# Kernel optimization log

Measured on AMD Instinct MI355X. Metric: run time of the kernel, lower is better.

The kernel has to match this reference:

```python
import jax, jax.numpy as jnp
import numpy as np

D_MODEL = 512
WINDOW = 128
N_HEADS = 8


def setup_inputs() -> dict:
    key = jax.random.key(0)
    k1, k2, k3, k4, k5 = jax.random.split(key, 5)
    B, S, D = 8, 4096, D_MODEL
    scale = 1.0 / np.sqrt(D)
    return {
        "x": jax.random.normal(k1, (B, S, D), dtype=jnp.float32),
        "in_proj_w": jax.random.normal(k2, (3 * D, D), dtype=jnp.float32) * scale,
        "in_proj_b": jax.random.normal(k3, (3 * D,), dtype=jnp.float32) * 0.02,
        "out_proj_w": jax.random.normal(k4, (D, D), dtype=jnp.float32) * scale,
        "out_proj_b": jax.random.normal(k5, (D,), dtype=jnp.float32) * 0.02,
    }


def reference(x, in_proj_w, in_proj_b, out_proj_w, out_proj_b):
    # Non-overlapping sliding-window MHA with shared weights per window.
    B, S, D = x.shape
    W = WINDOW
    H = N_HEADS
    hd = D // H
    nw = S // W  # S chosen divisible by window size

    xw = x.reshape(B, nw, W, D)
    # Fused QKV projection (torch in_proj_weight layout: [3D, D], y = x @ W^T + b)
    qkv = jnp.einsum("bnwd,ed->bnwe", xw, in_proj_w) + in_proj_b  # [B,nw,W,3D]
    q, k, v = jnp.split(qkv, 3, axis=-1)

    def to_heads(t):
        return t.reshape(B, nw, W, H, hd)

    q = to_heads(q) * (1.0 / np.sqrt(hd))
    k = to_heads(k)
    v = to_heads(v)

    # Block-diagonal attention: scores only within each window [B,nw,H,W,W]
    scores = jnp.einsum("bnqhd,bnkhd->bnhqk", q, k)
    attn = jax.nn.softmax(scores, axis=-1)
    ctx = jnp.einsum("bnhqk,bnkhd->bnqhd", attn, v)  # [B,nw,W,H,hd]
    ctx = ctx.reshape(B, S, D)

    out = jnp.einsum("bsd,ed->bse", ctx, out_proj_w) + out_proj_b
    return out
```

## Files before the change

### kernel.cpp

```cpp
#include <hip/hip_runtime.h>


typedef __bf16 bf16x8 __attribute__((ext_vector_type(8)));
typedef __bf16 bf16x4 __attribute__((ext_vector_type(4)));
typedef float  f32x4  __attribute__((ext_vector_type(4)));

#define MFMA16(a, b, c) __builtin_amdgcn_mfma_f32_16x16x32_bf16((a), (b), (c), 0, 0, 0)
#define VMCNT_(n) asm volatile("s_waitcnt vmcnt(" #n ")" ::: "memory")
#define VMCNT(n) VMCNT_(n)
#define LGKM0() asm volatile("s_waitcnt lgkmcnt(0)" ::: "memory")

__device__ __forceinline__ void gload_lds16(const __bf16* g, void* l) {
    __builtin_amdgcn_global_load_lds(
        (const __attribute__((address_space(1))) unsigned int*)g,
        (__attribute__((address_space(3))) unsigned int*)l, 16, 0, 0);
}

__device__ __forceinline__ void cvt8(const float* __restrict__ s,
                                     __bf16* __restrict__ d, long i) {
    const float4* s4 = reinterpret_cast<const float4*>(s);
    float4 a = s4[2 * i], b = s4[2 * i + 1];
    bf16x8 v;
    v[0] = (__bf16)a.x; v[1] = (__bf16)a.y; v[2] = (__bf16)a.z; v[3] = (__bf16)a.w;
    v[4] = (__bf16)b.x; v[5] = (__bf16)b.y; v[6] = (__bf16)b.z; v[7] = (__bf16)b.w;
    *reinterpret_cast<bf16x8*>(d + 8 * i) = v;
}

__global__ void convert_k(const float* __restrict__ x,
                          const float* __restrict__ w_in,
                          const float* __restrict__ w_out,
                          __bf16* __restrict__ x_bf,
                          __bf16* __restrict__ w_in_bf,
                          __bf16* __restrict__ w_out_bf)
{
    long i0 = (long)blockIdx.x * blockDim.x + threadIdx.x;
    long stride = (long)gridDim.x * blockDim.x;
    for (long i = i0; i < 16777216 / 8; i += stride) cvt8(x, x_bf, i);
    for (long i = i0; i < 786432 / 8;   i += stride) cvt8(w_in, w_in_bf, i);
    for (long i = i0; i < 262144 / 8;   i += stride) cvt8(w_out, w_out_bf, i);
}

template<int EPI, int NN>
__global__ __launch_bounds__(512, 2)
void gemm256(const __bf16* __restrict__ A,
             const __bf16* __restrict__ Bw,
             const float* __restrict__ bias,
             void* __restrict__ Cq,
             __bf16* __restrict__ vT)
{
    __shared__ __align__(16) char smem[65536];

    const int nwg = gridDim.x;
    const int chunk = nwg >> 3;
    const int bid = blockIdx.x;
    const int wg = (bid & 7) * chunk + (bid >> 3);
    const int nidx = wg % NN;
    const int midx = wg / NN;
    const long mbase = (long)midx * 256;
    const int colbase = nidx * 256;

    const int tid = threadIdx.x;
    const int w = tid >> 6, lane = tid & 63;
    const int lrow = lane & 15, hi = lane >> 4;
    const int wm = w >> 2, wn = w & 3;

    const int srow = tid >> 2;
    const int kchunk = (tid & 3) ^ ((srow >> 1) & 3);
    const __bf16* PA = A  + (mbase + srow) * 512 + kchunk * 8;
    const __bf16* PB = Bw + ((long)colbase + srow) * 512 + kchunk * 8;
    const int rd16 = (hi ^ ((lrow >> 1) & 3)) << 4;

    auto stage = [&](int t) {
        char* Ab = smem + (t & 1) * 16384;
        char* Bb = smem + 32768 + (t & 1) * 16384;
        const int ko = t * 32;
        gload_lds16(PA + ko,             Ab + w * 1024);
        gload_lds16(PA + 128 * 512 + ko, Ab + 8192 + w * 1024);
        gload_lds16(PB + ko,             Bb + w * 1024);
        gload_lds16(PB + 128 * 512 + ko, Bb + 8192 + w * 1024);
    };

    f32x4 acc[8][4];
    #pragma unroll
    for (int rt = 0; rt < 8; ++rt)
        #pragma unroll
        for (int ct = 0; ct < 4; ++ct) acc[rt][ct] = (f32x4){0.f, 0.f, 0.f, 0.f};

    stage(0);

    #pragma unroll 1
    for (int t = 0; t < 16; ++t) {
        VMCNT(0);
        LGKM0();
        __builtin_amdgcn_s_barrier();
        if (t < 15) stage(t + 1);
        const char* Ab = smem + (t & 1) * 16384;
        const char* Bb = smem + 32768 + (t & 1) * 16384;
        bf16x8 af[4], bfr[4];
        #pragma unroll
        for (int ct = 0; ct < 4; ++ct)
            bfr[ct] = *reinterpret_cast<const bf16x8*>(
                Bb + (64 * wn + 16 * ct + lrow) * 64 + rd16);
        #pragma unroll
        for (int i = 0; i < 4; ++i)
            af[i] = *reinterpret_cast<const bf16x8*>(
                Ab + (128 * wm + 16 * i + lrow) * 64 + rd16);
        __builtin_amdgcn_s_setprio(1);
        #pragma unroll
        for (int i = 0; i < 4; ++i)
            #pragma unroll
            for (int ct = 0; ct < 4; ++ct)
                acc[i][ct] = MFMA16(af[i], bfr[ct], acc[i][ct]);
        __builtin_amdgcn_s_setprio(0);
        #pragma unroll
        for (int i = 0; i < 4; ++i)
            af[i] = *reinterpret_cast<const bf16x8*>(
                Ab + (128 * wm + 64 + 16 * i + lrow) * 64 + rd16);
        __builtin_amdgcn_s_setprio(1);
        #pragma unroll
        for (int i = 0; i < 4; ++i)
            #pragma unroll
            for (int ct = 0; ct < 4; ++ct)
                acc[4 + i][ct] = MFMA16(af[i], bfr[ct], acc[4 + i][ct]);
        __builtin_amdgcn_s_setprio(0);
    }

    if (EPI == 0) {
        if (colbase < 1024) {
            const float scale = (colbase < 512) ? 0.125f : 1.0f;
            __bf16* qk = (__bf16*)Cq;
            #pragma unroll
            for (int ct = 0; ct < 4; ++ct) {
                int colg = colbase + 64 * wn + 16 * ct + lrow;
                float b = bias[colg];
                #pragma unroll
                for (int rt = 0; rt < 8; ++rt) {
                    long row = mbase + 128 * wm + 16 * rt + 4 * hi;
                    #pragma unroll
                    for (int r = 0; r < 4; ++r)
                        qk[(row + r) * 1024 + colg] = (__bf16)((acc[rt][ct][r] + b) * scale);
                }
            }
        } else {
            #pragma unroll
            for (int ct = 0; ct < 4; ++ct) {
                int colg = colbase + 64 * wn + 16 * ct + lrow;
                float b = bias[colg];
                int e2 = colg - 1024;
                int h = e2 >> 6, d = e2 & 63;
                #pragma unroll
                for (int rt = 0; rt < 8; ++rt) {
                    long row = mbase + 128 * wm + 16 * rt + 4 * hi;
                    int win = (int)(row >> 7), tok0 = (int)(row & 127);
                    bf16x4 pk;
                    pk[0] = (__bf16)(acc[rt][ct][0] + b);
                    pk[1] = (__bf16)(acc[rt][ct][1] + b);
                    pk[2] = (__bf16)(acc[rt][ct][2] + b);
                    pk[3] = (__bf16)(acc[rt][ct][3] + b);
                    *reinterpret_cast<bf16x4*>(
                        vT + (((long)win * 8 + h) * 64 + d) * 128 + tok0) = pk;
                }
            }
        }
    } else {
        float* outp = (float*)Cq;
        #pragma unroll
        for (int ct = 0; ct < 4; ++ct) {
            int colg = colbase + 64 * wn + 16 * ct + lrow;
            float b = bias[colg];
            #pragma unroll
            for (int rt = 0; rt < 8; ++rt) {
                long row = mbase + 128 * wm + 16 * rt + 4 * hi;
                #pragma unroll
                for (int r = 0; r < 4; ++r)
                    outp[(row + r) * 512 + colg] = acc[rt][ct][r] + b;
            }
        }
    }
}

__global__ __launch_bounds__(256)
void swa_attn(const __bf16* __restrict__ qk,
              const __bf16* __restrict__ vT,
              __bf16* __restrict__ ctx)
{
    __shared__ __bf16 p_lds[4][32][136];

    const int bid = blockIdx.x;
    const int win = bid >> 3, h = bid & 7;
    const int tid = threadIdx.x;
    const int w = tid >> 6, lane = tid & 63;
    const int lrow = lane & 15, hi = lane >> 4;
    const long tokb = (long)win * 128;

    bf16x8 qa[2][2];
    #pragma unroll
    for (int rt = 0; rt < 2; ++rt)
        #pragma unroll
        for (int ks = 0; ks < 2; ++ks)
            qa[rt][ks] = *reinterpret_cast<const bf16x8*>(
                qk + (tokb + 32 * w + 16 * rt + lrow) * 1024 + h * 64 + ks * 32 + hi * 8);

    f32x4 s[2][8];
    #pragma unroll
    for (int rt = 0; rt < 2; ++rt)
        #pragma unroll
        for (int ct = 0; ct < 8; ++ct) s[rt][ct] = (f32x4){0.f, 0.f, 0.f, 0.f};
    #pragma unroll
    for (int ks = 0; ks < 2; ++ks) {
        #pragma unroll
        for (int ct = 0; ct < 8; ++ct) {
            bf16x8 kb = *reinterpret_cast<const bf16x8*>(
                qk + (tokb + 16 * ct + lrow) * 1024 + 512 + h * 64 + ks * 32 + hi * 8);
            s[0][ct] = MFMA16(qa[0][ks], kb, s[0][ct]);
            s[1][ct] = MFMA16(qa[1][ks], kb, s[1][ct]);
        }
    }

    float inv[2][4];
    #pragma unroll
    for (int rt = 0; rt < 2; ++rt) {
        #pragma unroll
        for (int r = 0; r < 4; ++r) {
            float m = s[rt][0][r];
            #pragma unroll
            for (int ct = 1; ct < 8; ++ct) m = fmaxf(m, s[rt][ct][r]);
            m = fmaxf(m, __shfl_xor(m, 1));
            m = fmaxf(m, __shfl_xor(m, 2));
            m = fmaxf(m, __shfl_xor(m, 4));
            m = fmaxf(m, __shfl_xor(m, 8));
            float sum = 0.f;
            #pragma unroll
            for (int ct = 0; ct < 8; ++ct) {
                float e = __expf(s[rt][ct][r] - m);
                sum += e;
                p_lds[w][16 * rt + 4 * hi + r][16 * ct + lrow] = (__bf16)e;
            }
            sum += __shfl_xor(sum, 1);
            sum += __shfl_xor(sum, 2);
            sum += __shfl_xor(sum, 4);
            sum += __shfl_xor(sum, 8);
            inv[rt][r] = 1.f / sum;
        }
    }

    f32x4 o[2][4];
    #pragma unroll
    for (int rt = 0; rt < 2; ++rt)
        #pragma unroll
        for (int ct = 0; ct < 4; ++ct) o[rt][ct] = (f32x4){0.f, 0.f, 0.f, 0.f};
    const __bf16* vb = vT + ((long)win * 8 + h) * 64 * 128;
    #pragma unroll
    for (int kt = 0; kt < 4; ++kt) {
        bf16x8 pa0 = *reinterpret_cast<const bf16x8*>(&p_lds[w][lrow][32 * kt + 8 * hi]);
        bf16x8 pa1 = *reinterpret_cast<const bf16x8*>(&p_lds[w][16 + lrow][32 * kt + 8 * hi]);
        #pragma unroll
        for (int ct = 0; ct < 4; ++ct) {
            bf16x8 vf = *reinterpret_cast<const bf16x8*>(
                vb + (16 * ct + lrow) * 128 + 32 * kt + 8 * hi);
            o[0][ct] = MFMA16(pa0, vf, o[0][ct]);
            o[1][ct] = MFMA16(pa1, vf, o[1][ct]);
        }
    }

    #pragma unroll
    for (int rt = 0; rt < 2; ++rt)
        #pragma unroll
        for (int ct = 0; ct < 4; ++ct)
            #pragma unroll
            for (int r = 0; r < 4; ++r) {
                long tok = tokb + 32 * w + 16 * rt + 4 * hi + r;
                ctx[tok * 512 + h * 64 + 16 * ct + lrow] =
                    (__bf16)(o[rt][ct][r] * inv[rt][r]);
            }
}

extern "C" void kernel_launch(void* const* d_in, const int* in_sizes, int n_in,
                              void* d_out, int out_size, void* d_ws, size_t ws_size,
                              hipStream_t stream)
{
    const float* x     = (const float*)d_in[0];
    const float* w_in  = (const float*)d_in[1];
    const float* b_in  = (const float*)d_in[2];
    const float* w_out = (const float*)d_in[3];
    const float* b_out = (const float*)d_in[4];

    char* ws = (char*)d_ws;
    __bf16* x_bf     = (__bf16*)(ws);
    __bf16* ctx      = (__bf16*)(ws);
    __bf16* vT       = (__bf16*)(ws + 33554432);
    __bf16* w_in_bf  = (__bf16*)(ws + 67108864);
    __bf16* w_out_bf = (__bf16*)(ws + 68681728);
    __bf16* qk       = (__bf16*)d_out;

    convert_k<<<2048, 256, 0, stream>>>(x, w_in, w_out, x_bf, w_in_bf, w_out_bf);
    gemm256<0, 6><<<768, 512, 0, stream>>>(x_bf, w_in_bf, b_in, (void*)qk, vT);
    swa_attn<<<2048, 256, 0, stream>>>(qk, vT, ctx);
    gemm256<1, 2><<<256, 512, 0, stream>>>(ctx, w_out_bf, b_out, d_out, nullptr);
}
```

Before: 165.9 us.

## Use 256x128 GEMM tiles with triple-buffered LDS and staged coalesced epilogue

Shrinks the GEMM workgroup to 256 threads with a 256x128 output tile, which doubles the grid to 1536 and 512 blocks. The K loop now uses a three-slot LDS ring with prefetch distance two and a partial vmcnt wait, so global loads overlap with MFMA work instead of being drained every step. The QK and V^T epilogues are staged through swizzled LDS, so global writes become full 16-byte coalesced rows in place of scattered 2-byte and 8-byte stores. The cost is more LDS per block (72 KB), extra barriers, and each block re-reading the A tile because of the narrower N tile.

```diff
diff --git a/kernel.cpp b/kernel.cpp
--- a/kernel.cpp
+++ b/kernel.cpp
@@ -9,6 +9,7 @@
 #define VMCNT_(n) asm volatile("s_waitcnt vmcnt(" #n ")" ::: "memory")
 #define VMCNT(n) VMCNT_(n)
 #define LGKM0() asm volatile("s_waitcnt lgkmcnt(0)" ::: "memory")
+#define BAR() __builtin_amdgcn_s_barrier()
 
 __device__ __forceinline__ void gload_lds16(const __bf16* g, void* l) {
     __builtin_amdgcn_global_load_lds(
@@ -41,14 +42,14 @@
 }
 
 template<int EPI, int NN>
-__global__ __launch_bounds__(512, 2)
-void gemm256(const __bf16* __restrict__ A,
-             const __bf16* __restrict__ Bw,
-             const float* __restrict__ bias,
-             void* __restrict__ Cq,
-             __bf16* __restrict__ vT)
+__global__ __launch_bounds__(256, 2)
+void gemmT(const __bf16* __restrict__ A,
+           const __bf16* __restrict__ Bw,
+           const float* __restrict__ bias,
+           void* __restrict__ Cq,
+           __bf16* __restrict__ vT)
 {
-    __shared__ __align__(16) char smem[65536];
+    __shared__ __align__(16) char smem[73728];
 
     const int nwg = gridDim.x;
     const int chunk = nwg >> 3;
@@ -57,12 +58,12 @@
     const int nidx = wg % NN;
     const int midx = wg / NN;
     const long mbase = (long)midx * 256;
-    const int colbase = nidx * 256;
+    const int colbase = nidx * 128;
 
     const int tid = threadIdx.x;
     const int w = tid >> 6, lane = tid & 63;
     const int lrow = lane & 15, hi = lane >> 4;
-    const int wm = w >> 2, wn = w & 3;
+    const int wm = w >> 1, wn = w & 1;
 
     const int srow = tid >> 2;
     const int kchunk = (tid & 3) ^ ((srow >> 1) & 3);
@@ -70,14 +71,16 @@
     const __bf16* PB = Bw + ((long)colbase + srow) * 512 + kchunk * 8;
     const int rd16 = (hi ^ ((lrow >> 1) & 3)) << 4;
 
-    auto stage = [&](int t) {
-        char* Ab = smem + (t & 1) * 16384;
-        char* Bb = smem + 32768 + (t & 1) * 16384;
+    auto stage = [&](int t, int slot) {
+        char* Ab = smem + slot * 24576;
+        char* Bb = Ab + 16384;
         const int ko = t * 32;
-        gload_lds16(PA + ko,             Ab + w * 1024);
-        gload_lds16(PA + 128 * 512 + ko, Ab + 8192 + w * 1024);
-        gload_lds16(PB + ko,             Bb + w * 1024);
-        gload_lds16(PB + 128 * 512 + ko, Bb + 8192 + w * 1024);
+        #pragma unroll
+        for (int j = 0; j < 4; ++j)
+            gload_lds16(PA + (64 * j) * 512 + ko, Ab + j * 4096 + w * 1024);
+        #pragma unroll
+        for (int j = 0; j < 2; ++j)
+            gload_lds16(PB + (64 * j) * 512 + ko, Bb + j * 4096 + w * 1024);
     };
 
     f32x4 acc[8][4];
@@ -86,16 +89,18 @@
         #pragma unroll
         for (int ct = 0; ct < 4; ++ct) acc[rt][ct] = (f32x4){0.f, 0.f, 0.f, 0.f};
 
-    stage(0);
-
+    stage(0, 0); stage(1, 1);
+
+    int cs = 0;
+    int ss = 2;
     #pragma unroll 1
     for (int t = 0; t < 16; ++t) {
-        VMCNT(0);
+        if (t < 15) { VMCNT(6); } else { VMCNT(0); }
         LGKM0();
-        __builtin_amdgcn_s_barrier();
-        if (t < 15) stage(t + 1);
-        const char* Ab = smem + (t & 1) * 16384;
-        const char* Bb = smem + 32768 + (t & 1) * 16384;
+        BAR();
+        if (t < 14) stage(t + 2, ss);
+        const char* Ab = smem + cs * 24576;
+        const char* Bb = Ab + 16384;
         bf16x8 af[4], bfr[4];
         #pragma unroll
         for (int ct = 0; ct < 4; ++ct)
@@ -123,7 +128,11 @@
             for (int ct = 0; ct < 4; ++ct)
                 acc[4 + i][ct] = MFMA16(af[i], bfr[ct], acc[4 + i][ct]);
         __builtin_amdgcn_s_setprio(0);
-    }
+        cs = (cs == 2) ? 0 : cs + 1;
+        ss = (ss == 2) ? 0 : ss + 1;
+    }
+    LGKM0();
+    BAR();
 
     if (EPI == 0) {
         if (colbase < 1024) {
@@ -131,35 +140,56 @@
             __bf16* qk = (__bf16*)Cq;
             #pragma unroll
             for (int ct = 0; ct < 4; ++ct) {
-                int colg = colbase + 64 * wn + 16 * ct + lrow;
-                float b = bias[colg];
+                int col = 64 * wn + 16 * ct + lrow;
+                float b = bias[colbase + col];
+                #pragma unroll
+                for (int rt = 0; rt < 8; ++rt)
+                    #pragma unroll
+                    for (int r = 0; r < 4; ++r) {
+                        int row = 128 * wm + 16 * rt + 4 * hi + r;
+                        *reinterpret_cast<__bf16*>(
+                            smem + row * 256 + ((col * 2) ^ ((row & 15) << 4))) =
+                            (__bf16)((acc[rt][ct][r] + b) * scale);
+                    }
+            }
+            LGKM0();
+            BAR();
+            #pragma unroll
+            for (int i = 0; i < 16; ++i) {
+                int row = 16 * i + (tid >> 4);
+                int slot = (tid & 15) ^ (tid >> 4);
+                bf16x8 v = *reinterpret_cast<const bf16x8*>(smem + row * 256 + slot * 16);
+                *reinterpret_cast<bf16x8*>(
+                    qk + (mbase + row) * 1024 + colbase + (tid & 15) * 8) = v;
+            }
+        } else {
+            #pragma unroll
+            for (int ct = 0; ct < 4; ++ct) {
+                int e = 64 * wn + 16 * ct + lrow;
+                float b = bias[colbase + e];
                 #pragma unroll
                 for (int rt = 0; rt < 8; ++rt) {
-                    long row = mbase + 128 * wm + 16 * rt + 4 * hi;
-                    #pragma unroll
-                    for (int r = 0; r < 4; ++r)
-                        qk[(row + r) * 1024 + colg] = (__bf16)((acc[rt][ct][r] + b) * scale);
-                }
-            }
-        } else {
-            #pragma unroll
-            for (int ct = 0; ct < 4; ++ct) {
-                int colg = colbase + 64 * wn + 16 * ct + lrow;
-                float b = bias[colg];
-                int e2 = colg - 1024;
-                int h = e2 >> 6, d = e2 & 63;
-                #pragma unroll
-                for (int rt = 0; rt < 8; ++rt) {
-                    long row = mbase + 128 * wm + 16 * rt + 4 * hi;
-                    int win = (int)(row >> 7), tok0 = (int)(row & 127);
+                    int tok0 = 128 * wm + 16 * rt + 4 * hi;
                     bf16x4 pk;
                     pk[0] = (__bf16)(acc[rt][ct][0] + b);
                     pk[1] = (__bf16)(acc[rt][ct][1] + b);
                     pk[2] = (__bf16)(acc[rt][ct][2] + b);
                     pk[3] = (__bf16)(acc[rt][ct][3] + b);
                     *reinterpret_cast<bf16x4*>(
-                        vT + (((long)win * 8 + h) * 64 + d) * 128 + tok0) = pk;
+                        smem + e * 512 + ((tok0 * 2) ^ ((e & 15) << 4))) = pk;
                 }
+            }
+            LGKM0();
+            BAR();
+            #pragma unroll
+            for (int i = 0; i < 16; ++i) {
+                int e = 8 * i + (tid >> 5);
+                int gch = tid & 31;
+                int slot = gch ^ (e & 15);
+                bf16x8 v = *reinterpret_cast<const bf16x8*>(smem + e * 512 + slot * 16);
+                long win = 2 * midx + (gch >> 4);
+                *reinterpret_cast<bf16x8*>(
+                    vT + (win * 512 + (colbase - 1024 + e)) * 128 + (gch & 15) * 8) = v;
             }
         }
     } else {
@@ -249,7 +279,7 @@
     for (int rt = 0; rt < 2; ++rt)
         #pragma unroll
         for (int ct = 0; ct < 4; ++ct) o[rt][ct] = (f32x4){0.f, 0.f, 0.f, 0.f};
-    const __bf16* vb = vT + ((long)win * 8 + h) * 64 * 128;
+    const __bf16* vb = vT + (long)win * 512 * 128 + (long)h * 64 * 128;
     #pragma unroll
     for (int kt = 0; kt < 4; ++kt) {
         bf16x8 pa0 = *reinterpret_cast<const bf16x8*>(&p_lds[w][lrow][32 * kt + 8 * hi]);
@@ -294,7 +324,7 @@
     __bf16* qk       = (__bf16*)d_out;
 
     convert_k<<<2048, 256, 0, stream>>>(x, w_in, w_out, x_bf, w_in_bf, w_out_bf);
-    gemm256<0, 6><<<768, 512, 0, stream>>>(x_bf, w_in_bf, b_in, (void*)qk, vT);
+    gemmT<0, 12><<<1536, 256, 0, stream>>>(x_bf, w_in_bf, b_in, (void*)qk, vT);
     swa_attn<<<2048, 256, 0, stream>>>(qk, vT, ctx);
-    gemm256<1, 2><<<256, 512, 0, stream>>>(ctx, w_out_bf, b_out, d_out, nullptr);
-}
+    gemmT<1, 4><<<512, 256, 0, stream>>>(ctx, w_out_bf, b_out, d_out, nullptr);
+}
```

Result: faster. 160.0 us (-3.5%).

## Shrink GEMM tiles to 256x128 with 4 waves and swizzle attention block order

Applied to the files above, without the earlier changes.

The GEMM kernel moves from 256x256 tiles with 512 threads to 256x128 tiles with 256 threads. LDS use drops to 48KB and the launch bound is set to 3 blocks per CU, so the grid doubles, which should give better CU fill and occupancy on both projections. The attention kernel remaps block indices so consecutive blocks are spread across chunks, which may improve cache or XCD locality. The trade-off is less operand reuse per tile, meaning more global and LDS traffic per FLOP.

```diff
diff --git a/kernel.cpp b/kernel.cpp
--- a/kernel.cpp
+++ b/kernel.cpp
@@ -9,6 +9,7 @@
 #define VMCNT_(n) asm volatile("s_waitcnt vmcnt(" #n ")" ::: "memory")
 #define VMCNT(n) VMCNT_(n)
 #define LGKM0() asm volatile("s_waitcnt lgkmcnt(0)" ::: "memory")
+#define BAR() __builtin_amdgcn_s_barrier()
 
 __device__ __forceinline__ void gload_lds16(const __bf16* g, void* l) {
     __builtin_amdgcn_global_load_lds(
@@ -41,14 +42,14 @@
 }
 
 template<int EPI, int NN>
-__global__ __launch_bounds__(512, 2)
-void gemm256(const __bf16* __restrict__ A,
-             const __bf16* __restrict__ Bw,
-             const float* __restrict__ bias,
-             void* __restrict__ Cq,
-             __bf16* __restrict__ vT)
+__global__ __launch_bounds__(256, 3)
+void gemmT(const __bf16* __restrict__ A,
+           const __bf16* __restrict__ Bw,
+           const float* __restrict__ bias,
+           void* __restrict__ Cq,
+           __bf16* __restrict__ vT)
 {
-    __shared__ __align__(16) char smem[65536];
+    __shared__ __align__(16) char smem[49152];
 
     const int nwg = gridDim.x;
     const int chunk = nwg >> 3;
@@ -57,12 +58,12 @@
     const int nidx = wg % NN;
     const int midx = wg / NN;
     const long mbase = (long)midx * 256;
-    const int colbase = nidx * 256;
+    const int colbase = nidx * 128;
 
     const int tid = threadIdx.x;
     const int w = tid >> 6, lane = tid & 63;
     const int lrow = lane & 15, hi = lane >> 4;
-    const int wm = w >> 2, wn = w & 3;
+    const int wm = w >> 1, wn = w & 1;
 
     const int srow = tid >> 2;
     const int kchunk = (tid & 3) ^ ((srow >> 1) & 3);
@@ -71,13 +72,15 @@
     const int rd16 = (hi ^ ((lrow >> 1) & 3)) << 4;
 
     auto stage = [&](int t) {
-        char* Ab = smem + (t & 1) * 16384;
-        char* Bb = smem + 32768 + (t & 1) * 16384;
+        char* Ab = smem + (t & 1) * 24576;
+        char* Bb = Ab + 16384;
         const int ko = t * 32;
-        gload_lds16(PA + ko,             Ab + w * 1024);
-        gload_lds16(PA + 128 * 512 + ko, Ab + 8192 + w * 1024);
-        gload_lds16(PB + ko,             Bb + w * 1024);
-        gload_lds16(PB + 128 * 512 + ko, Bb + 8192 + w * 1024);
+        #pragma unroll
+        for (int j = 0; j < 4; ++j)
+            gload_lds16(PA + (64 * j) * 512 + ko, Ab + j * 4096 + w * 1024);
+        #pragma unroll
+        for (int j = 0; j < 2; ++j)
+            gload_lds16(PB + (64 * j) * 512 + ko, Bb + j * 4096 + w * 1024);
     };
 
     f32x4 acc[8][4];
@@ -92,10 +95,10 @@
     for (int t = 0; t < 16; ++t) {
         VMCNT(0);
         LGKM0();
-        __builtin_amdgcn_s_barrier();
+        BAR();
         if (t < 15) stage(t + 1);
-        const char* Ab = smem + (t & 1) * 16384;
-        const char* Bb = smem + 32768 + (t & 1) * 16384;
+        const char* Ab = smem + (t & 1) * 24576;
+        const char* Bb = Ab + 16384;
         bf16x8 af[4], bfr[4];
         #pragma unroll
         for (int ct = 0; ct < 4; ++ct)
@@ -146,8 +149,7 @@
             for (int ct = 0; ct < 4; ++ct) {
                 int colg = colbase + 64 * wn + 16 * ct + lrow;
                 float b = bias[colg];
-                int e2 = colg - 1024;
-                int h = e2 >> 6, d = e2 & 63;
+                int e = colg - 1024;
                 #pragma unroll
                 for (int rt = 0; rt < 8; ++rt) {
                     long row = mbase + 128 * wm + 16 * rt + 4 * hi;
@@ -158,7 +160,7 @@
                     pk[2] = (__bf16)(acc[rt][ct][2] + b);
                     pk[3] = (__bf16)(acc[rt][ct][3] + b);
                     *reinterpret_cast<bf16x4*>(
-                        vT + (((long)win * 8 + h) * 64 + d) * 128 + tok0) = pk;
+                        vT + ((long)win * 512 + e) * 128 + tok0) = pk;
                 }
             }
         }
@@ -187,7 +189,8 @@
     __shared__ __bf16 p_lds[4][32][136];
 
     const int bid = blockIdx.x;
-    const int win = bid >> 3, h = bid & 7;
+    const int wg = (bid & 7) * 256 + (bid >> 3);
+    const int win = wg >> 3, h = wg & 7;
     const int tid = threadIdx.x;
     const int w = tid >> 6, lane = tid & 63;
     const int lrow = lane & 15, hi = lane >> 4;
@@ -249,7 +252,7 @@
     for (int rt = 0; rt < 2; ++rt)
         #pragma unroll
         for (int ct = 0; ct < 4; ++ct) o[rt][ct] = (f32x4){0.f, 0.f, 0.f, 0.f};
-    const __bf16* vb = vT + ((long)win * 8 + h) * 64 * 128;
+    const __bf16* vb = vT + (long)win * 512 * 128 + (long)h * 64 * 128;
     #pragma unroll
     for (int kt = 0; kt < 4; ++kt) {
         bf16x8 pa0 = *reinterpret_cast<const bf16x8*>(&p_lds[w][lrow][32 * kt + 8 * hi]);
@@ -294,7 +297,7 @@
     __bf16* qk       = (__bf16*)d_out;
 
     convert_k<<<2048, 256, 0, stream>>>(x, w_in, w_out, x_bf, w_in_bf, w_out_bf);
-    gemm256<0, 6><<<768, 512, 0, stream>>>(x_bf, w_in_bf, b_in, (void*)qk, vT);
+    gemmT<0, 12><<<1536, 256, 0, stream>>>(x_bf, w_in_bf, b_in, (void*)qk, vT);
     swa_attn<<<2048, 256, 0, stream>>>(qk, vT, ctx);
-    gemm256<1, 2><<<256, 512, 0, stream>>>(ctx, w_out_bf, b_out, d_out, nullptr);
-}
+    gemmT<1, 4><<<512, 256, 0, stream>>>(ctx, w_out_bf, b_out, d_out, nullptr);
+}
```

Result: slower. 194.0 us (+17.0%).
